# Kernel tuning notes

Hardware: AMD Instinct MI355X
Metric: run time of the kernel (lower is better)

## Reference

```python
import jax, jax.numpy as jnp
import numpy as np

D = 1024
W_SIZE = 512
K_ENGRAMS = 16
REPEAT = W_SIZE // K_ENGRAMS  # 32
LN_EPS = 1e-5


def setup_inputs() -> dict:
    key = jax.random.key(0)
    ks = jax.random.split(key, 6)
    B, NW = 4, 16
    engrams = jax.random.normal(ks[0], (B, NW, K_ENGRAMS, D), dtype=jnp.float32)
    pos_emb = 0.02 * jax.random.normal(ks[1], (1, 1, W_SIZE, D), dtype=jnp.float32)
    w1 = 0.02 * jax.random.normal(ks[2], (D, D), dtype=jnp.float32)
    b1 = jnp.zeros((D,), dtype=jnp.float32)
    w2 = 0.02 * jax.random.normal(ks[3], (D, D), dtype=jnp.float32)
    b2 = jnp.zeros((D,), dtype=jnp.float32)
    gamma = jnp.ones((D,), dtype=jnp.float32)
    beta = jnp.zeros((D,), dtype=jnp.float32)
    return {"engrams": engrams, "pos_emb": pos_emb, "w1": w1, "b1": b1,
            "w2": w2, "b2": b2, "gamma": gamma, "beta": beta}


def reference(engrams, pos_emb, w1, b1, w2, b2, gamma, beta):
    # (B, nw, K, d) -> (B, nw, W, d) via repeat_interleave along axis 2
    x = jnp.repeat(engrams, REPEAT, axis=2) + pos_emb
    # refine MLP: Linear -> GELU (exact) -> Linear, with residual
    h = jax.nn.gelu(jnp.einsum('bnwd,de->bnwe', x, w1.T) + b1, approximate=False)
    x = x + jnp.einsum('bnwd,de->bnwe', h, w2.T) + b2
    # LayerNorm over last dim
    mu = jnp.mean(x, axis=-1, keepdims=True)
    var = jnp.mean(jnp.square(x - mu), axis=-1, keepdims=True)
    return (x - mu) * jax.lax.rsqrt(var + LN_EPS) * gamma + beta
```

## Files before the change

kernel.cpp:

```cpp
#include <hip/hip_runtime.h>
#include <hip/hip_bf16.h>
#include <math.h>

#define D_DIM 1024
#define NROWS 32768
#define NE_ROWS 1024
#define A1_ROWS 1536

typedef __attribute__((ext_vector_type(8))) short bf16x8;
typedef __attribute__((ext_vector_type(4))) float f32x4;

static __device__ __forceinline__ ushort f2bf(float f) {
  union { float f; unsigned u; } un; un.f = f;
  unsigned u = un.u;
  unsigned r = u + 0x7fffu + ((u >> 16) & 1u);
  return (ushort)(r >> 16);
}

__global__ void cast_kernel(const float* __restrict__ src, ushort* __restrict__ dst, int n4) {
  int i = blockIdx.x * blockDim.x + threadIdx.x;
  if (i >= n4) return;
  float4 v = ((const float4*)src)[i];
  ushort4 o;
  o.x = f2bf(v.x); o.y = f2bf(v.y); o.z = f2bf(v.z); o.w = f2bf(v.w);
  ((ushort4*)dst)[i] = o;
}

__global__ __launch_bounds__(256) void gemm_bt(const ushort* __restrict__ A,
                                               const ushort* __restrict__ B,
                                               float* __restrict__ C,
                                               int M, int N, int K) {
  __shared__ ushort sA[128 * 64];
  __shared__ ushort sB[128 * 64];

  int nwg = gridDim.x;
  int bid = blockIdx.x;
  if ((nwg & 7) == 0) {
    int cpx = nwg >> 3;
    bid = (bid & 7) * cpx + (bid >> 3);
  }
  int ntn = N >> 7;
  int mt = bid / ntn, nt = bid % ntn;
  int brow = mt << 7, bcol = nt << 7;

  int tid = threadIdx.x;
  int wv = tid >> 6, lane = tid & 63;
  int wm = (wv >> 1) << 6, wn = (wv & 1) << 6;
  int lr = lane & 15, lk = lane >> 4;
  int srow = lane >> 3, scol = (lane & 7) << 3;

  f32x4 acc[4][4];
#pragma unroll
  for (int m = 0; m < 4; ++m)
#pragma unroll
    for (int n = 0; n < 4; ++n) acc[m][n] = (f32x4){0.f, 0.f, 0.f, 0.f};

  for (int k0 = 0; k0 < K; k0 += 64) {
    __syncthreads();
#pragma unroll
    for (int j = 0; j < 4; ++j) {
      int c = (wv << 2) + j;
      int row = (c << 3) + srow;
      const ushort* gA = A + (brow + row) * K + k0 + scol;
      const ushort* gB = B + (bcol + row) * K + k0 + scol;
      __builtin_amdgcn_global_load_lds(
          (const __attribute__((address_space(1))) unsigned int*)gA,
          (__attribute__((address_space(3))) unsigned int*)&sA[c << 9], 16, 0, 0);
      __builtin_amdgcn_global_load_lds(
          (const __attribute__((address_space(1))) unsigned int*)gB,
          (__attribute__((address_space(3))) unsigned int*)&sB[c << 9], 16, 0, 0);
    }
    __syncthreads();
#pragma unroll
    for (int kk = 0; kk < 2; ++kk) {
      bf16x8 af[4], bfr[4];
#pragma unroll
      for (int m = 0; m < 4; ++m)
        af[m] = *(const bf16x8*)&sA[(wm + (m << 4) + lr) * 64 + (kk << 5) + (lk << 3)];
#pragma unroll
      for (int n = 0; n < 4; ++n)
        bfr[n] = *(const bf16x8*)&sB[(wn + (n << 4) + lr) * 64 + (kk << 5) + (lk << 3)];
#pragma unroll
      for (int m = 0; m < 4; ++m)
#pragma unroll
        for (int n = 0; n < 4; ++n)
          acc[m][n] = __builtin_amdgcn_mfma_f32_16x16x32_bf16(af[m], bfr[n], acc[m][n], 0, 0, 0);
    }
  }

#pragma unroll
  for (int m = 0; m < 4; ++m)
#pragma unroll
    for (int n = 0; n < 4; ++n)
#pragma unroll
      for (int i = 0; i < 4; ++i) {
        int row = brow + wm + (m << 4) + (lk << 2) + i;
        int col = bcol + wn + (n << 4) + lr;
        C[(long)row * N + col] = acc[m][n][i];
      }
}

__global__ __launch_bounds__(256) void gelu_kernel(const float* __restrict__ xw1,
                                                   const float* __restrict__ b1,
                                                   ushort* __restrict__ h) {
  int r = blockIdx.x;
  int t = threadIdx.x;
  int bn = r >> 9;
  int w = r & 511;
  int er = bn * 16 + (w >> 5);
  float4 e = ((const float4*)(xw1 + er * D_DIM))[t];
  float4 p = ((const float4*)(xw1 + (NE_ROWS + w) * D_DIM))[t];
  float4 b = ((const float4*)b1)[t];
  float v[4] = {e.x + p.x + b.x, e.y + p.y + b.y, e.z + p.z + b.z, e.w + p.w + b.w};
  ushort4 o;
  float g0 = 0.5f * v[0] * (1.0f + erff(v[0] * 0.70710678118654752f));
  float g1 = 0.5f * v[1] * (1.0f + erff(v[1] * 0.70710678118654752f));
  float g2 = 0.5f * v[2] * (1.0f + erff(v[2] * 0.70710678118654752f));
  float g3 = 0.5f * v[3] * (1.0f + erff(v[3] * 0.70710678118654752f));
  o.x = f2bf(g0); o.y = f2bf(g1); o.z = f2bf(g2); o.w = f2bf(g3);
  ((ushort4*)(h + (long)r * D_DIM))[t] = o;
}

__global__ __launch_bounds__(256) void ln_kernel(const float* __restrict__ eng,
                                                 const float* __restrict__ pos,
                                                 const float* __restrict__ b2,
                                                 const float* __restrict__ gamma,
                                                 const float* __restrict__ beta,
                                                 float* __restrict__ out) {
  __shared__ float red[8];
  int r = blockIdx.x;
  int t = threadIdx.x;
  int bn = r >> 9, w = r & 511;
  int er = bn * 16 + (w >> 5);
  float4 xe = ((const float4*)(eng + er * D_DIM))[t];
  float4 xp = ((const float4*)(pos + w * D_DIM))[t];
  float4 y  = ((const float4*)(out + (long)r * D_DIM))[t];
  float4 bb = ((const float4*)b2)[t];
  float v0 = xe.x + xp.x + y.x + bb.x;
  float v1 = xe.y + xp.y + y.y + bb.y;
  float v2 = xe.z + xp.z + y.z + bb.z;
  float v3 = xe.w + xp.w + y.w + bb.w;
  float s  = v0 + v1 + v2 + v3;
  float sq = v0 * v0 + v1 * v1 + v2 * v2 + v3 * v3;
  int lane = t & 63, wv = t >> 6;
#pragma unroll
  for (int off = 32; off > 0; off >>= 1) {
    s  += __shfl_down(s, off);
    sq += __shfl_down(sq, off);
  }
  if (lane == 0) { red[wv] = s; red[4 + wv] = sq; }
  __syncthreads();
  float S  = red[0] + red[1] + red[2] + red[3];
  float SQ = red[4] + red[5] + red[6] + red[7];
  float mu = S * (1.0f / 1024.0f);
  float var = SQ * (1.0f / 1024.0f) - mu * mu;
  float rs = rsqrtf(var + 1e-5f);
  float4 g = ((const float4*)gamma)[t];
  float4 bt = ((const float4*)beta)[t];
  float4 o;
  o.x = (v0 - mu) * rs * g.x + bt.x;
  o.y = (v1 - mu) * rs * g.y + bt.y;
  o.z = (v2 - mu) * rs * g.z + bt.z;
  o.w = (v3 - mu) * rs * g.w + bt.w;
  ((float4*)(out + (long)r * D_DIM))[t] = o;
}

extern "C" void kernel_launch(void* const* d_in, const int* in_sizes, int n_in,
                              void* d_out, int out_size, void* d_ws, size_t ws_size,
                              hipStream_t stream) {
  const float* eng   = (const float*)d_in[0];
  const float* pos   = (const float*)d_in[1];
  const float* w1    = (const float*)d_in[2];
  const float* b1    = (const float*)d_in[3];
  const float* w2    = (const float*)d_in[4];
  const float* b2    = (const float*)d_in[5];
  const float* gamma = (const float*)d_in[6];
  const float* beta  = (const float*)d_in[7];
  float* out = (float*)d_out;

  char* ws = (char*)d_ws;
  ushort* w1b = (ushort*)(ws);
  ushort* w2b = (ushort*)(ws + (2u << 20));
  ushort* a1b = (ushort*)(ws + (4u << 20));
  float*  xw1 = (float*)(ws + (7u << 20));
  ushort* hb  = (ushort*)(ws + (13u << 20));

  cast_kernel<<<1024, 256, 0, stream>>>(w1, w1b, 1024 * 1024 / 4);
  cast_kernel<<<1024, 256, 0, stream>>>(w2, w2b, 1024 * 1024 / 4);
  cast_kernel<<<1024, 256, 0, stream>>>(eng, a1b, 1024 * 1024 / 4);
  cast_kernel<<<512, 256, 0, stream>>>(pos, a1b + 1024 * 1024, 512 * 1024 / 4);

  gemm_bt<<<(A1_ROWS / 128) * (D_DIM / 128), 256, 0, stream>>>(a1b, w1b, xw1,
                                                               A1_ROWS, D_DIM, D_DIM);

  gelu_kernel<<<NROWS, 256, 0, stream>>>(xw1, b1, hb);

  gemm_bt<<<(NROWS / 128) * (D_DIM / 128), 256, 0, stream>>>(hb, w2b, out,
                                                             NROWS, D_DIM, D_DIM);

  ln_kernel<<<NROWS, 256, 0, stream>>>(eng, pos, b2, gamma, beta, out);
}
```

Before: 211.0 us.

## Add pipelined 256x256 GEMM2 with bf16 output, LDS swizzle, and fused casts

Replaces the second GEMM with a 512-thread kernel using 256x256 tiles, double-buffered global-to-LDS loads interleaved with MFMA phases, and setprio hints. Its output is written as bf16 into the output buffer and read back by layernorm, which halves that intermediate's traffic but adds bf16 rounding before the residual. It also adds an XOR swizzle to LDS layouts in the first GEMM to cut bank conflicts, and merges the four cast launches into one. The hand-placed waitcnt and barrier schedule is fragile.

```diff
diff --git a/kernel.cpp b/kernel.cpp
--- a/kernel.cpp
+++ b/kernel.cpp
@@ -6,6 +6,7 @@
 #define NROWS 32768
 #define NE_ROWS 1024
 #define A1_ROWS 1536
+#define NT2 16
 
 typedef __attribute__((ext_vector_type(8))) short bf16x8;
 typedef __attribute__((ext_vector_type(4))) float f32x4;
@@ -16,11 +17,23 @@
   unsigned r = u + 0x7fffu + ((u >> 16) & 1u);
   return (ushort)(r >> 16);
 }
-
-__global__ void cast_kernel(const float* __restrict__ src, ushort* __restrict__ dst, int n4) {
+static __device__ __forceinline__ float bf2f(ushort h) {
+  union { unsigned u; float f; } un; un.u = ((unsigned)h) << 16;
+  return un.f;
+}
+static __device__ __forceinline__ float gelu_exact(float v) {
+  return 0.5f * v * (1.0f + erff(v * 0.70710678118654752f));
+}
+
+__global__ void cast_all_kernel(const float* __restrict__ w1, const float* __restrict__ w2,
+                                const float* __restrict__ eng, const float* __restrict__ pos,
+                                ushort* __restrict__ dst) {
   int i = blockIdx.x * blockDim.x + threadIdx.x;
-  if (i >= n4) return;
-  float4 v = ((const float4*)src)[i];
+  float4 v;
+  if (i < 262144) v = ((const float4*)w1)[i];
+  else if (i < 524288) v = ((const float4*)w2)[i - 262144];
+  else if (i < 786432) v = ((const float4*)eng)[i - 524288];
+  else v = ((const float4*)pos)[i - 786432];
   ushort4 o;
   o.x = f2bf(v.x); o.y = f2bf(v.y); o.z = f2bf(v.z); o.w = f2bf(v.w);
   ((ushort4*)dst)[i] = o;
@@ -47,7 +60,8 @@
   int wv = tid >> 6, lane = tid & 63;
   int wm = (wv >> 1) << 6, wn = (wv & 1) << 6;
   int lr = lane & 15, lk = lane >> 4;
-  int srow = lane >> 3, scol = (lane & 7) << 3;
+  int srow = lane >> 3;
+  int scolsw = (((lane & 7) ^ ((lane >> 3) & 7)) << 3);
 
   f32x4 acc[4][4];
 #pragma unroll
@@ -61,8 +75,8 @@
     for (int j = 0; j < 4; ++j) {
       int c = (wv << 2) + j;
       int row = (c << 3) + srow;
-      const ushort* gA = A + (brow + row) * K + k0 + scol;
-      const ushort* gB = B + (bcol + row) * K + k0 + scol;
+      const ushort* gA = A + (brow + row) * K + k0 + scolsw;
+      const ushort* gB = B + (bcol + row) * K + k0 + scolsw;
       __builtin_amdgcn_global_load_lds(
           (const __attribute__((address_space(1))) unsigned int*)gA,
           (__attribute__((address_space(3))) unsigned int*)&sA[c << 9], 16, 0, 0);
@@ -73,13 +87,14 @@
     __syncthreads();
 #pragma unroll
     for (int kk = 0; kk < 2; ++kk) {
+      int rdoff = (((kk << 2) | lk) ^ (lr & 7)) << 3;
       bf16x8 af[4], bfr[4];
 #pragma unroll
       for (int m = 0; m < 4; ++m)
-        af[m] = *(const bf16x8*)&sA[(wm + (m << 4) + lr) * 64 + (kk << 5) + (lk << 3)];
+        af[m] = *(const bf16x8*)&sA[(wm + (m << 4) + lr) * 64 + rdoff];
 #pragma unroll
       for (int n = 0; n < 4; ++n)
-        bfr[n] = *(const bf16x8*)&sB[(wn + (n << 4) + lr) * 64 + (kk << 5) + (lk << 3)];
+        bfr[n] = *(const bf16x8*)&sB[(wn + (n << 4) + lr) * 64 + rdoff];
 #pragma unroll
       for (int m = 0; m < 4; ++m)
 #pragma unroll
@@ -111,14 +126,121 @@
   float4 e = ((const float4*)(xw1 + er * D_DIM))[t];
   float4 p = ((const float4*)(xw1 + (NE_ROWS + w) * D_DIM))[t];
   float4 b = ((const float4*)b1)[t];
-  float v[4] = {e.x + p.x + b.x, e.y + p.y + b.y, e.z + p.z + b.z, e.w + p.w + b.w};
   ushort4 o;
-  float g0 = 0.5f * v[0] * (1.0f + erff(v[0] * 0.70710678118654752f));
-  float g1 = 0.5f * v[1] * (1.0f + erff(v[1] * 0.70710678118654752f));
-  float g2 = 0.5f * v[2] * (1.0f + erff(v[2] * 0.70710678118654752f));
-  float g3 = 0.5f * v[3] * (1.0f + erff(v[3] * 0.70710678118654752f));
-  o.x = f2bf(g0); o.y = f2bf(g1); o.z = f2bf(g2); o.w = f2bf(g3);
+  o.x = f2bf(gelu_exact(e.x + p.x + b.x));
+  o.y = f2bf(gelu_exact(e.y + p.y + b.y));
+  o.z = f2bf(gelu_exact(e.z + p.z + b.z));
+  o.w = f2bf(gelu_exact(e.w + p.w + b.w));
   ((ushort4*)(h + (long)r * D_DIM))[t] = o;
+}
+
+__global__ __launch_bounds__(512, 2) void gemm2_8ph(const ushort* __restrict__ A,
+                                                    const ushort* __restrict__ B,
+                                                    ushort* __restrict__ Y) {
+  __shared__ ushort sA[2][2][8192];
+  __shared__ ushort sB[2][2][8192];
+  const int K = 1024;
+
+  int bid = blockIdx.x;
+  bid = (bid & 7) * 64 + (bid >> 3);
+  int mt = bid >> 2, nt = bid & 3;
+  long brow = (long)mt << 8;
+  int bcol = nt << 8;
+
+  int tid = threadIdx.x;
+  int wv = tid >> 6, l = tid & 63;
+  int wr = wv >> 2, wc = wv & 3;
+  int lr = l & 15, lk = l >> 4;
+
+  int sr = (wv << 4) + (l >> 2);
+  int slog = ((l & 3) ^ ((l >> 3) & 3)) << 3;
+  const ushort* aS = A + (brow + sr) * (long)K + slog;
+  const ushort* bS = B + (size_t)(bcol + sr) * K + slog;
+
+  int rdswz = (lk ^ ((lr >> 1) & 3)) << 3;
+  int aO = (((wr << 7) + lr) << 5) + rdswz;
+  int bO = (((wc << 6) + lr) << 5) + rdswz;
+
+  f32x4 acc[8][4];
+#pragma unroll
+  for (int m = 0; m < 8; ++m)
+#pragma unroll
+    for (int n = 0; n < 4; ++n) acc[m][n] = (f32x4){0.f, 0.f, 0.f, 0.f};
+
+#define STG(SS, SRC, kt, kkh) do {                                                   \
+    int p_ = (kt) & 1; int o_ = ((kt) << 6) + ((kkh) << 5);                          \
+    __builtin_amdgcn_global_load_lds(                                                \
+      (const __attribute__((address_space(1))) unsigned int*)((SRC) + o_),           \
+      (__attribute__((address_space(3))) unsigned int*)&SS[p_][kkh][wv << 9], 16, 0, 0); \
+    __builtin_amdgcn_global_load_lds(                                                \
+      (const __attribute__((address_space(1))) unsigned int*)((SRC) + o_ + 131072),  \
+      (__attribute__((address_space(3))) unsigned int*)&SS[p_][kkh][(wv << 9) + 4096], 16, 0, 0); \
+  } while (0)
+
+#define BAR asm volatile("s_barrier" ::: "memory")
+#define MFMA16(MOFS, BF)                                                             \
+    __builtin_amdgcn_s_setprio(1);                                                   \
+    _Pragma("unroll")                                                                \
+    for (int m = 0; m < 4; ++m)                                                      \
+      _Pragma("unroll")                                                              \
+      for (int n = 0; n < 4; ++n)                                                    \
+        acc[m + MOFS][n] = __builtin_amdgcn_mfma_f32_16x16x32_bf16(af[m], BF[n], acc[m + MOFS][n], 0, 0, 0); \
+    __builtin_amdgcn_s_setprio(0)
+
+  STG(sA, aS, 0, 0); STG(sB, bS, 0, 0); STG(sA, aS, 0, 1); STG(sB, bS, 0, 1);
+  asm volatile("s_waitcnt vmcnt(0)" ::: "memory");
+  BAR;
+
+  for (int t = 0; t < NT2; ++t) {
+    int p = t & 1;
+    bf16x8 af[4], bf[4];
+#pragma unroll
+    for (int n = 0; n < 4; ++n) bf[n] = *(const bf16x8*)&sB[p][0][bO + (n << 9)];
+#pragma unroll
+    for (int m = 0; m < 4; ++m) af[m] = *(const bf16x8*)&sA[p][0][aO + (m << 9)];
+    if (t + 1 < NT2) STG(sA, aS, t + 1, 0);
+    BAR;
+    MFMA16(0, bf);
+    BAR;
+#pragma unroll
+    for (int m = 0; m < 4; ++m) af[m] = *(const bf16x8*)&sA[p][0][aO + ((m + 4) << 9)];
+    if (t + 1 < NT2) STG(sB, bS, t + 1, 0);
+    BAR;
+    MFMA16(4, bf);
+    if (t == NT2 - 1) asm volatile("s_waitcnt vmcnt(0)" ::: "memory");
+    else              asm volatile("s_waitcnt vmcnt(4)" ::: "memory");
+    BAR;
+#pragma unroll
+    for (int n = 0; n < 4; ++n) bf[n] = *(const bf16x8*)&sB[p][1][bO + (n << 9)];
+#pragma unroll
+    for (int m = 0; m < 4; ++m) af[m] = *(const bf16x8*)&sA[p][1][aO + (m << 9)];
+    if (t + 1 < NT2) STG(sA, aS, t + 1, 1);
+    BAR;
+    MFMA16(0, bf);
+    BAR;
+#pragma unroll
+    for (int m = 0; m < 4; ++m) af[m] = *(const bf16x8*)&sA[p][1][aO + ((m + 4) << 9)];
+    if (t + 1 < NT2) STG(sB, bS, t + 1, 1);
+    BAR;
+    MFMA16(4, bf);
+    if (t < NT2 - 1) asm volatile("s_waitcnt vmcnt(4)" ::: "memory");
+    BAR;
+  }
+#undef STG
+#undef BAR
+#undef MFMA16
+
+#pragma unroll
+  for (int m = 0; m < 8; ++m)
+#pragma unroll
+    for (int n = 0; n < 4; ++n) {
+      int col = bcol + (wc << 6) + (n << 4) + lr;
+#pragma unroll
+      for (int i = 0; i < 4; ++i) {
+        long row = brow + (wr << 7) + (m << 4) + (lk << 2) + i;
+        Y[(row << 11) + col] = f2bf(acc[m][n][i]);
+      }
+    }
 }
 
 __global__ __launch_bounds__(256) void ln_kernel(const float* __restrict__ eng,
@@ -134,12 +256,12 @@
   int er = bn * 16 + (w >> 5);
   float4 xe = ((const float4*)(eng + er * D_DIM))[t];
   float4 xp = ((const float4*)(pos + w * D_DIM))[t];
-  float4 y  = ((const float4*)(out + (long)r * D_DIM))[t];
+  ushort4 yv = ((const ushort4*)((const ushort*)out + ((size_t)r << 11)))[t];
   float4 bb = ((const float4*)b2)[t];
-  float v0 = xe.x + xp.x + y.x + bb.x;
-  float v1 = xe.y + xp.y + y.y + bb.y;
-  float v2 = xe.z + xp.z + y.z + bb.z;
-  float v3 = xe.w + xp.w + y.w + bb.w;
+  float v0 = xe.x + xp.x + bf2f(yv.x) + bb.x;
+  float v1 = xe.y + xp.y + bf2f(yv.y) + bb.y;
+  float v2 = xe.z + xp.z + bf2f(yv.z) + bb.z;
+  float v3 = xe.w + xp.w + bf2f(yv.w) + bb.w;
   float s  = v0 + v1 + v2 + v3;
   float sq = v0 * v0 + v1 * v1 + v2 * v2 + v3 * v3;
   int lane = t & 63, wv = t >> 6;
@@ -162,7 +284,7 @@
   o.y = (v1 - mu) * rs * g.y + bt.y;
   o.z = (v2 - mu) * rs * g.z + bt.z;
   o.w = (v3 - mu) * rs * g.w + bt.w;
-  ((float4*)(out + (long)r * D_DIM))[t] = o;
+  ((float4*)(out + ((size_t)r << 10)))[t] = o;
 }
 
 extern "C" void kernel_launch(void* const* d_in, const int* in_sizes, int n_in,
@@ -185,18 +307,14 @@
   float*  xw1 = (float*)(ws + (7u << 20));
   ushort* hb  = (ushort*)(ws + (13u << 20));
 
-  cast_kernel<<<1024, 256, 0, stream>>>(w1, w1b, 1024 * 1024 / 4);
-  cast_kernel<<<1024, 256, 0, stream>>>(w2, w2b, 1024 * 1024 / 4);
-  cast_kernel<<<1024, 256, 0, stream>>>(eng, a1b, 1024 * 1024 / 4);
-  cast_kernel<<<512, 256, 0, stream>>>(pos, a1b + 1024 * 1024, 512 * 1024 / 4);
+  cast_all_kernel<<<3584, 256, 0, stream>>>(w1, w2, eng, pos, w1b);
 
   gemm_bt<<<(A1_ROWS / 128) * (D_DIM / 128), 256, 0, stream>>>(a1b, w1b, xw1,
                                                                A1_ROWS, D_DIM, D_DIM);
 
   gelu_kernel<<<NROWS, 256, 0, stream>>>(xw1, b1, hb);
 
-  gemm_bt<<<(NROWS / 128) * (D_DIM / 128), 256, 0, stream>>>(hb, w2b, out,
-                                                             NROWS, D_DIM, D_DIM);
+  gemm2_8ph<<<512, 512, 0, stream>>>(hb, w2b, (ushort*)out);
 
   ln_kernel<<<NROWS, 256, 0, stream>>>(eng, pos, b2, gamma, beta, out);
 }
```

After: 173.1 us. -18.0%, faster.
